# Performance work log

Measured on AMD Instinct MI355X. Metric: run time of the kernel, lower is better.

## Reference

```python
import jax, jax.numpy as jnp
import numpy as np

P, V, GRID = 64, 6890, 32
V_SUB = 256          # vertex subsample for the SDF-grid proxy
SCALE_FACTOR = 0.2   # forward() default
SDF_BAND = 0.15      # proxy: phi = relu(band - dist_to_surface) >= 0
N_FACES = 13776


def _trilinear(vol, pts):
    """torch grid_sample 3D, mode=bilinear, padding=zeros, align_corners=False.
    vol: [D,H,W]; pts: [...,3] with (x,y,z) in [-1,1] mapping to (W,H,D)."""
    D, H, W = vol.shape
    x = ((pts[..., 0] + 1.0) * W - 1.0) * 0.5
    y = ((pts[..., 1] + 1.0) * H - 1.0) * 0.5
    z = ((pts[..., 2] + 1.0) * D - 1.0) * 0.5
    x0 = jnp.floor(x).astype(jnp.int32); fx = x - x0
    y0 = jnp.floor(y).astype(jnp.int32); fy = y - y0
    z0 = jnp.floor(z).astype(jnp.int32); fz = z - z0

    def corner(xi, yi, zi, w):
        inb = (xi >= 0) & (xi < W) & (yi >= 0) & (yi < H) & (zi >= 0) & (zi < D)
        v = vol[jnp.clip(zi, 0, D - 1), jnp.clip(yi, 0, H - 1), jnp.clip(xi, 0, W - 1)]
        return jnp.where(inb, v, 0.0) * w

    return (corner(x0,     y0,     z0,     (1 - fx) * (1 - fy) * (1 - fz))
          + corner(x0 + 1, y0,     z0,     fx       * (1 - fy) * (1 - fz))
          + corner(x0,     y0 + 1, z0,     (1 - fx) * fy       * (1 - fz))
          + corner(x0 + 1, y0 + 1, z0,     fx       * fy       * (1 - fz))
          + corner(x0,     y0,     z0 + 1, (1 - fx) * (1 - fy) * fz)
          + corner(x0 + 1, y0,     z0 + 1, fx       * (1 - fy) * fz)
          + corner(x0,     y0 + 1, z0 + 1, (1 - fx) * fy       * fz)
          + corner(x0 + 1, y0 + 1, z0 + 1, fx       * fy       * fz))


def _compute_phi(verts_cs):
    """Deterministic non-negative SDF-grid proxy (stands in for the external
    SDF CUDA op; original computes it under no_grad). verts_cs: [P,V,3] in [-1,1].
    Returns phi: [P,GRID,GRID,GRID] (D,H,W indexing)."""
    # cell centers in normalized coords (align_corners=False convention)
    lin = (2.0 * jnp.arange(GRID, dtype=verts_cs.dtype) + 1.0) / GRID - 1.0
    zz, yy, xx = jnp.meshgrid(lin, lin, lin, indexing='ij')
    gp = jnp.stack([xx, yy, zz], axis=-1).reshape(-1, 3)  # [G^3,3] (x,y,z)
    stride = V // V_SUB
    sub = verts_cs[:, ::stride, :][:, :V_SUB]             # [P,V_SUB,3]

    def per_person(v):  # v: [V_SUB,3]
        d2 = jnp.sum((gp[:, None, :] - v[None, :, :]) ** 2, axis=-1)  # [G^3,V_SUB]
        d = jnp.sqrt(jnp.min(d2, axis=-1))
        return jnp.maximum(SDF_BAND - d, 0.0).reshape(GRID, GRID, GRID)

    return jax.lax.map(per_person, sub)  # sequential over people: bounds peak memory


def _forward(vertices, translation):
    sg = jax.lax.stop_gradient
    verts = vertices + translation[:, None, :]                      # [P,V,3]
    n = verts.shape[0]
    bmin = sg(jnp.min(verts, axis=1))                               # [P,3] (no_grad bboxes)
    bmax = sg(jnp.max(verts, axis=1))
    # overlap(i,j) per axis: not (min_i > max_j or min_j > max_i)
    ov = jnp.all((bmin[:, None, :] <= bmax[None, :, :]) &
                 (bmin[None, :, :] <= bmax[:, None, :]), axis=-1)   # [P,P], diag True
    # faithful to original ~filter_isolated_boxes: kept only if overlapping ALL others
    valid = jnp.all(ov, axis=1)                                     # [P]
    nv = jnp.sum(valid.astype(verts.dtype))
    center = (bmin + bmax) * 0.5                                    # [P,3]
    scale = (1.0 + SCALE_FACTOR) * 0.5 * jnp.max(bmax - bmin, axis=-1)  # [P]
    verts_cs = sg((verts - center[:, None, :]) / scale[:, None, None])
    phi = sg(_compute_phi(verts_cs))                                # [P,G,G,G]
    # coordinates of ALL people's vertices in person-i's grid frame: [P,P,V,3]
    loc = (verts[None, :, :, :] - center[:, None, None, :]) / scale[:, None, None, None]
    phi_val = jax.vmap(_trilinear)(phi, loc.reshape(n, n * V, 3)).reshape(n, n, V)
    # pair (i,j) contributes iff both valid and i != j (weights[i]=0 in the loop)
    pair_w = (valid[:, None] & valid[None, :] & ~jnp.eye(n, dtype=bool)).astype(verts.dtype)
    denom = jnp.maximum(nv, 1.0) ** 2
    return jnp.sum(pair_w * jnp.sum(phi_val, axis=-1)) / denom


def setup_inputs() -> dict:
    key = jax.random.key(0)
    k1, k2, k3 = jax.random.split(key, 3)
    vertices = jax.random.normal(k1, (P, V, 3), dtype=jnp.float32) * 0.2
    translation = jax.random.uniform(k2, (P, 3), dtype=jnp.float32, minval=-0.3, maxval=0.3)
    faces = jax.random.randint(k3, (N_FACES, 3), 0, V, dtype=jnp.int32)
    return {"vertices": vertices, "translation": translation, "faces": faces}


def reference(vertices, translation, faces):
    # faces only feed the external SDF op (replaced by the phi proxy); unused here
    return _forward(vertices, translation)
```

## Files before the change

kernel.cpp:

```cpp
#include <hip/hip_runtime.h>


#define NP 64
#define NVERT 6890
#define NV3 (NVERT*3)
#define GRD 32
#define QDIM 34
#define QPLANE (QDIM*QDIM)
#define QVOL (QDIM*QPLANE)
#define VSUB 256
#define VSTRIDE 26
#define BAND 0.15f
#define PHI_SCALE 64.0f
#define INV_PHI_SCALE 0.015625f
#define LDS_BYTES (QVOL*2 + 64)
#define SAMPLE_BLOCKS (4*NP)

typedef float floatx2 __attribute__((ext_vector_type(2)));

__device__ __forceinline__ float wave_min(float v) {
  #pragma unroll
  for (int off = 32; off > 0; off >>= 1) v = fminf(v, __shfl_down(v, off));
  return v;
}
__device__ __forceinline__ float wave_max(float v) {
  #pragma unroll
  for (int off = 32; off > 0; off >>= 1) v = fmaxf(v, __shfl_down(v, off));
  return v;
}
__device__ __forceinline__ float wave_sum(float v) {
  #pragma unroll
  for (int off = 32; off > 0; off >>= 1) v += __shfl_down(v, off);
  return v;
}

__global__ __launch_bounds__(1024) void k_soa_bounds(
    const float* __restrict__ verts, const float* __restrict__ trans,
    float* __restrict__ vertsT, float* __restrict__ bbox,
    float* __restrict__ accp, unsigned int* __restrict__ donep) {
  int p = blockIdx.x;
  int tid = threadIdx.x;
  if (p == 0 && tid == 0) { accp[0] = 0.0f; donep[0] = 0u; }
  const float* vp = verts + (size_t)p * NV3;
  float tx = trans[p*3+0], ty = trans[p*3+1], tz = trans[p*3+2];
  float* o0 = vertsT + (size_t)(p*3+0) * NVERT;
  float* o1 = vertsT + (size_t)(p*3+1) * NVERT;
  float* o2 = vertsT + (size_t)(p*3+2) * NVERT;
  float mnx=1e30f, mny=1e30f, mnz=1e30f, mxx=-1e30f, mxy=-1e30f, mxz=-1e30f;
  for (int t2 = tid; t2 < NVERT/2; t2 += 1024) {
    const float* b = vp + t2*6;
    floatx2 A = *(const floatx2*)(b);
    floatx2 B = *(const floatx2*)(b+2);
    floatx2 C = *(const floatx2*)(b+4);
    mnx=fminf(mnx,fminf(A.x,B.y)); mxx=fmaxf(mxx,fmaxf(A.x,B.y));
    mny=fminf(mny,fminf(A.y,C.x)); mxy=fmaxf(mxy,fmaxf(A.y,C.x));
    mnz=fminf(mnz,fminf(B.x,C.y)); mxz=fmaxf(mxz,fmaxf(B.x,C.y));
    floatx2 sx = {A.x+tx, B.y+tx};
    floatx2 sy = {A.y+ty, C.x+ty};
    floatx2 sz = {B.x+tz, C.y+tz};
    *(floatx2*)(o0 + 2*t2) = sx;
    *(floatx2*)(o1 + 2*t2) = sy;
    *(floatx2*)(o2 + 2*t2) = sz;
  }
  mnx=wave_min(mnx)+tx; mny=wave_min(mny)+ty; mnz=wave_min(mnz)+tz;
  mxx=wave_max(mxx)+tx; mxy=wave_max(mxy)+ty; mxz=wave_max(mxz)+tz;
  __shared__ float s[16][6];
  int wave = tid >> 6, lane = tid & 63;
  if (lane == 0) {
    s[wave][0]=mnx; s[wave][1]=mny; s[wave][2]=mnz;
    s[wave][3]=mxx; s[wave][4]=mxy; s[wave][5]=mxz;
  }
  __syncthreads();
  if (tid == 0) {
    float a0=s[0][0],a1=s[0][1],a2=s[0][2],b0=s[0][3],b1=s[0][4],b2=s[0][5];
    for (int w = 1; w < 16; ++w) {
      a0=fminf(a0,s[w][0]); a1=fminf(a1,s[w][1]); a2=fminf(a2,s[w][2]);
      b0=fmaxf(b0,s[w][3]); b1=fmaxf(b1,s[w][4]); b2=fmaxf(b2,s[w][5]);
    }
    bbox[p*3+0]=a0; bbox[p*3+1]=a1; bbox[p*3+2]=a2;
    bbox[192+p*3+0]=b0; bbox[192+p*3+1]=b1; bbox[192+p*3+2]=b2;
  }
}

__global__ __launch_bounds__(1024) void k_phi(
    const float* __restrict__ verts, const float* __restrict__ trans,
    const float* __restrict__ bbox, unsigned short* __restrict__ pairs,
    float* __restrict__ centerg,
    float* __restrict__ validg, int* __restrict__ jlistg,
    int* __restrict__ jcountg, float* __restrict__ nvg) {
  int p = blockIdx.x >> 2;
  int zq = blockIdx.x & 3;
  int tid = threadIdx.x;
  int x = tid & 31, y = tid >> 5;

  __shared__ float kv[VSUB][3];
  __shared__ float phib[8][32][32];
  __shared__ int nkeep;

  const float inv = 1.0f / (float)GRD;
  if (tid == 0) nkeep = 0;
  __syncthreads();

  float bx0 = bbox[p*3+0], by0 = bbox[p*3+1], bz0 = bbox[p*3+2];
  float bx1 = bbox[192+p*3+0], by1 = bbox[192+p*3+1], bz1 = bbox[192+p*3+2];
  float cx = 0.5f*(bx0+bx1), cy = 0.5f*(by0+by1), cz = 0.5f*(bz0+bz1);
  float ext = fmaxf(bx1-bx0, fmaxf(by1-by0, bz1-bz0));
  float is = 1.0f / (0.6f * ext);

  if (zq == 0 && tid == 0) {
    centerg[p*4+0] = cx; centerg[p*4+1] = cy; centerg[p*4+2] = cz;
    centerg[p*4+3] = is * 16.0f;
  }
  if (blockIdx.x == 0 && tid < 64) {
    bool valid = true;
    for (int j = 0; j < NP; ++j) {
      bool ov = true;
      #pragma unroll
      for (int c = 0; c < 3; ++c)
        ov = ov && (bbox[tid*3+c] <= bbox[192+j*3+c]) &&
                   (bbox[j*3+c] <= bbox[192+tid*3+c]);
      valid = valid && ov;
    }
    unsigned long long mm = __ballot(valid);
    if (valid) {
      int pos = (int)__popcll(mm & ((1ull << tid) - 1ull));
      jlistg[pos] = tid;
    }
    validg[tid] = valid ? 1.0f : 0.0f;
    if (tid == 0) {
      jcountg[0] = (int)__popcll(mm);
      nvg[0] = (float)__popcll(mm);
    }
  }

  if (tid < VSUB) {
    int v = tid * VSTRIDE;
    const float* vp = verts + (size_t)p * NV3 + (size_t)v * 3;
    float X = (vp[0] + trans[p*3+0] - cx) * is;
    float Y = (vp[1] + trans[p*3+1] - cy) * is;
    float Z = (vp[2] + trans[p*3+2] - cz) * is;
    float zlo = (2.0f*(zq*8)     + 1.0f) * inv - 1.0f;
    float zhi = (2.0f*(zq*8 + 7) + 1.0f) * inv - 1.0f;
    float dz = fmaxf(fmaxf(zlo - Z, Z - zhi), 0.0f);
    if (dz < BAND) {
      int idx = atomicAdd(&nkeep, 1);
      kv[idx][0] = X; kv[idx][1] = Y; kv[idx][2] = Z;
    }
  }
  __syncthreads();
  int nk = nkeep;

  float gx = (2.0f*x + 1.0f) * inv - 1.0f;
  float gy = (2.0f*y + 1.0f) * inv - 1.0f;
  float gz[8];
  #pragma unroll
  for (int k = 0; k < 8; ++k) gz[k] = (2.0f*(zq*8+k) + 1.0f) * inv - 1.0f;

  float d2[8];
  #pragma unroll
  for (int k = 0; k < 8; ++k) d2[k] = 1e30f;

  int w = tid >> 6;
  float ylo = (4.0f*w + 1.0f) * inv - 1.0f;
  float yhi = (4.0f*w + 3.0f) * inv - 1.0f;

  for (int v = 0; v < nk; ++v) {
    float Y = kv[v][1];
    if (fmaxf(ylo - Y, Y - yhi) >= BAND) continue;
    float dx = gx - kv[v][0];
    float dy = gy - Y;
    float vzv = kv[v][2];
    float r2 = fmaf(dy, dy, dx*dx);
    #pragma unroll
    for (int k = 0; k < 8; ++k) {
      float dz = gz[k] - vzv;
      d2[k] = fminf(d2[k], fmaf(dz, dz, r2));
    }
  }
  #pragma unroll
  for (int k = 0; k < 8; ++k)
    phib[k][y][x] = fmaxf(BAND - sqrtf(d2[k]), 0.0f) * PHI_SCALE;
  __syncthreads();

  unsigned short* qp = pairs + (size_t)p * QVOL;
  for (int idx = tid; idx < QPLANE; idx += 1024) {
    int iy = idx / QDIM, ix = idx % QDIM;
    int gyy = iy - 1, gxx = ix - 1;
    bool gyok = (unsigned)gyy < 32u;
    bool aok = gyok && ((unsigned)gxx < 32u);
    bool bok = gyok && ((unsigned)ix  < 32u);
    int ya = gyok ? gyy : 0;
    int xa = aok ? gxx : 0;
    int xb = bok ? ix : 0;
    #pragma unroll
    for (int k = 0; k < 8; ++k) {
      float a = aok ? phib[k][ya][xa] : 0.0f;
      float b = bok ? phib[k][ya][xb] : 0.0f;
      int pk = __builtin_amdgcn_cvt_pk_fp8_f32(a, b, 0, false);
      qp[(zq*8 + k + 1)*QPLANE + idx] = (unsigned short)(pk & 0xffff);
    }
    if (zq == 0) qp[idx] = 0;
    if (zq == 3) qp[33*QPLANE + idx] = 0;
  }
}

__device__ __forceinline__ float qsample(const unsigned short* q,
                                         float X, float Y, float Z) {
  X = fminf(fmaxf(X, 0.0f), 33.99f);
  Y = fminf(fmaxf(Y, 0.0f), 32.999f);
  Z = fminf(fmaxf(Z, 0.0f), 32.999f);
  float xf = floorf(X), yf = floorf(Y), zf = floorf(Z);
  float fx = X - xf, fy = Y - yf, fz = Z - zf;
  int e = ((int)zf * QDIM + (int)yf) * QDIM + (int)xf;
  unsigned int w00 = q[e];
  unsigned int w10 = q[e + QDIM];
  unsigned int w01 = q[e + QPLANE];
  unsigned int w11 = q[e + QPLANE + QDIM];
  floatx2 c00 = __builtin_amdgcn_cvt_pk_f32_fp8((int)w00, false);
  floatx2 c10 = __builtin_amdgcn_cvt_pk_f32_fp8((int)w10, false);
  floatx2 c01 = __builtin_amdgcn_cvt_pk_f32_fp8((int)w01, false);
  floatx2 c11 = __builtin_amdgcn_cvt_pk_f32_fp8((int)w11, false);
  float u00 = fmaf(fx, c00.y - c00.x, c00.x);
  float u10 = fmaf(fx, c10.y - c10.x, c10.x);
  float u01 = fmaf(fx, c01.y - c01.x, c01.x);
  float u11 = fmaf(fx, c11.y - c11.x, c11.x);
  float a0 = fmaf(fy, u10 - u00, u00);
  float a1 = fmaf(fy, u11 - u01, u01);
  return fmaf(fz, a1 - a0, a0);
}

__global__ __launch_bounds__(896, 7) void k_sample(
    const float* __restrict__ vertsT, const float* __restrict__ centerg,
    const float* __restrict__ validg, const unsigned short* __restrict__ pairs,
    const int* __restrict__ jlistg, const int* __restrict__ jcountg,
    const float* __restrict__ nvg, float* __restrict__ accp,
    unsigned int* __restrict__ donep, float* __restrict__ out) {
  extern __shared__ unsigned char smem[];
  const unsigned short* sq = (const unsigned short*)smem;
  float* red = (float*)(smem + (size_t)QVOL * 2);

  int i = blockIdx.y;
  int tid = threadIdx.x;
  int njl = jcountg[0];

  if (validg[i] != 0.0f) {
    {
      const uint4* src = (const uint4*)(pairs + (size_t)i * QVOL);
      uint4* dst = (uint4*)smem;
      for (int t = tid; t < QVOL/8; t += 896) dst[t] = src[t];
    }
    __syncthreads();

    int v0 = blockIdx.x * 1792 + tid;
    int v1 = v0 + 896;
    bool ok1 = v1 < NVERT;
    int vc1 = ok1 ? v1 : 0;
    float s16 = centerg[i*4+3];
    float bx  = fmaf(-centerg[i*4+0], s16, 16.5f);
    float by  = fmaf(-centerg[i*4+1], s16, 16.5f);
    float bz  = fmaf(-centerg[i*4+2], s16, 16.5f);
    float bx1 = bx + (ok1 ? 0.0f : 1e9f);

    float acc = 0.0f;
    #pragma unroll 2
    for (int t = 0; t < njl; ++t) {
      int jj = jlistg[t];
      if (jj == i) continue;
      const float* p0 = vertsT + (size_t)(jj*3) * NVERT;
      float Xa = fmaf(p0[v0],          s16, bx);
      float Ya = fmaf(p0[NVERT+v0],    s16, by);
      float Za = fmaf(p0[2*NVERT+v0],  s16, bz);
      float Xb = fmaf(p0[vc1],         s16, bx1);
      float Yb = fmaf(p0[NVERT+vc1],   s16, by);
      float Zb = fmaf(p0[2*NVERT+vc1], s16, bz);
      acc += qsample(sq, Xa, Ya, Za);
      acc += qsample(sq, Xb, Yb, Zb);
    }

    acc = wave_sum(acc);
    int wv = tid >> 6, lane = tid & 63;
    if (lane == 0) red[wv] = acc;
    __syncthreads();
    if (tid == 0) {
      float tot = 0.0f;
      #pragma unroll
      for (int w = 0; w < 14; ++w) tot += red[w];
      atomicAdd(accp, tot * INV_PHI_SCALE);
    }
  }

  if (tid == 0) {
    __threadfence();
    unsigned int old = atomicAdd(donep, 1u);
    if (old == SAMPLE_BLOCKS - 1) {
      float nv = fmaxf(nvg[0], 1.0f);
      float loss = atomicAdd(accp, 0.0f);
      out[0] = loss / (nv * nv);
    }
  }
}

extern "C" void kernel_launch(void* const* d_in, const int* in_sizes, int n_in,
                              void* d_out, int out_size, void* d_ws, size_t ws_size,
                              hipStream_t stream) {
  const float* verts = (const float*)d_in[0];
  const float* trans = (const float*)d_in[1];
  float* out = (float*)d_out;

  unsigned short* pairs = (unsigned short*)d_ws;
  float* vertsT    = (float*)((unsigned char*)d_ws + (size_t)NP * QVOL * 2);
  float* bbox      = vertsT + (size_t)NP * NV3;
  float* centerg   = bbox + 384;
  float* validg    = centerg + NP*4;
  float* nvg       = validg + NP;
  float* accp      = nvg + 1;
  unsigned int* donep = (unsigned int*)(accp + 1);
  int* jlistg      = (int*)(donep + 1);
  int* jcountg     = jlistg + NP;

  hipFuncSetAttribute((const void*)k_sample,
                      hipFuncAttributeMaxDynamicSharedMemorySize, LDS_BYTES);

  k_soa_bounds<<<NP, 1024, 0, stream>>>(verts, trans, vertsT, bbox, accp, donep);
  k_phi<<<NP*4, 1024, 0, stream>>>(verts, trans, bbox, pairs, centerg,
                                   validg, jlistg, jcountg, nvg);
  k_sample<<<dim3(4, NP), 896, LDS_BYTES, stream>>>(vertsT, centerg, validg,
                                                    pairs, jlistg, jcountg,
                                                    nvg, accp, donep, out);
}
```

Baseline: 103.2 us.

## Pack 2x2 xy-quads of fp8 phi per dword to halve LDS gathers

The phi grid is now stored as one 32-bit word per cell holding the fp8 values of the 2x2 xy neighbourhood, instead of 16-bit x-pairs. Each trilinear sample therefore needs two LDS loads instead of four. k_phi is split into 8 z-slabs of 4 planes per person rather than 4 slabs of 8 planes. The cost is double the LDS footprint (about 157KB per block) and a doubled global staging copy, and the occupancy hint is dropped from the launch bounds.

```diff
diff --git a/kernel.cpp b/kernel.cpp
--- a/kernel.cpp
+++ b/kernel.cpp
@@ -13,7 +13,7 @@
 #define BAND 0.15f
 #define PHI_SCALE 64.0f
 #define INV_PHI_SCALE 0.015625f
-#define LDS_BYTES (QVOL*2 + 64)
+#define LDS_BYTES (QVOL*4 + 64)
 #define SAMPLE_BLOCKS (4*NP)
 
 typedef float floatx2 __attribute__((ext_vector_type(2)));
@@ -84,17 +84,17 @@
 
 __global__ __launch_bounds__(1024) void k_phi(
     const float* __restrict__ verts, const float* __restrict__ trans,
-    const float* __restrict__ bbox, unsigned short* __restrict__ pairs,
+    const float* __restrict__ bbox, unsigned int* __restrict__ quad,
     float* __restrict__ centerg,
     float* __restrict__ validg, int* __restrict__ jlistg,
     int* __restrict__ jcountg, float* __restrict__ nvg) {
-  int p = blockIdx.x >> 2;
-  int zq = blockIdx.x & 3;
+  int p = blockIdx.x >> 3;
+  int zq = blockIdx.x & 7;
   int tid = threadIdx.x;
   int x = tid & 31, y = tid >> 5;
 
   __shared__ float kv[VSUB][3];
-  __shared__ float phib[8][32][32];
+  __shared__ float phib[4][32][32];
   __shared__ int nkeep;
 
   const float inv = 1.0f / (float)GRD;
@@ -139,8 +139,8 @@
     float X = (vp[0] + trans[p*3+0] - cx) * is;
     float Y = (vp[1] + trans[p*3+1] - cy) * is;
     float Z = (vp[2] + trans[p*3+2] - cz) * is;
-    float zlo = (2.0f*(zq*8)     + 1.0f) * inv - 1.0f;
-    float zhi = (2.0f*(zq*8 + 7) + 1.0f) * inv - 1.0f;
+    float zlo = (2.0f*(zq*4)     + 1.0f) * inv - 1.0f;
+    float zhi = (2.0f*(zq*4 + 3) + 1.0f) * inv - 1.0f;
     float dz = fmaxf(fmaxf(zlo - Z, Z - zhi), 0.0f);
     if (dz < BAND) {
       int idx = atomicAdd(&nkeep, 1);
@@ -152,13 +152,13 @@
 
   float gx = (2.0f*x + 1.0f) * inv - 1.0f;
   float gy = (2.0f*y + 1.0f) * inv - 1.0f;
-  float gz[8];
-  #pragma unroll
-  for (int k = 0; k < 8; ++k) gz[k] = (2.0f*(zq*8+k) + 1.0f) * inv - 1.0f;
-
-  float d2[8];
-  #pragma unroll
-  for (int k = 0; k < 8; ++k) d2[k] = 1e30f;
+  float gz[4];
+  #pragma unroll
+  for (int k = 0; k < 4; ++k) gz[k] = (2.0f*(zq*4+k) + 1.0f) * inv - 1.0f;
+
+  float d2[4];
+  #pragma unroll
+  for (int k = 0; k < 4; ++k) d2[k] = 1e30f;
 
   int w = tid >> 6;
   float ylo = (4.0f*w + 1.0f) * inv - 1.0f;
@@ -172,72 +172,70 @@
     float vzv = kv[v][2];
     float r2 = fmaf(dy, dy, dx*dx);
     #pragma unroll
-    for (int k = 0; k < 8; ++k) {
+    for (int k = 0; k < 4; ++k) {
       float dz = gz[k] - vzv;
       d2[k] = fminf(d2[k], fmaf(dz, dz, r2));
     }
   }
   #pragma unroll
-  for (int k = 0; k < 8; ++k)
+  for (int k = 0; k < 4; ++k)
     phib[k][y][x] = fmaxf(BAND - sqrtf(d2[k]), 0.0f) * PHI_SCALE;
   __syncthreads();
 
-  unsigned short* qp = pairs + (size_t)p * QVOL;
+  unsigned int* qp = quad + (size_t)p * QVOL;
   for (int idx = tid; idx < QPLANE; idx += 1024) {
     int iy = idx / QDIM, ix = idx % QDIM;
     int gyy = iy - 1, gxx = ix - 1;
-    bool gyok = (unsigned)gyy < 32u;
-    bool aok = gyok && ((unsigned)gxx < 32u);
-    bool bok = gyok && ((unsigned)ix  < 32u);
-    int ya = gyok ? gyy : 0;
-    int xa = aok ? gxx : 0;
-    int xb = bok ? ix : 0;
+    bool x0ok = (unsigned)gxx < 32u, x1ok = (unsigned)ix < 32u;
+    bool y0ok = (unsigned)gyy < 32u, y1ok = (unsigned)iy < 32u;
+    int xa = x0ok ? gxx : 0, xb = x1ok ? ix : 0;
+    int ya = y0ok ? gyy : 0, yb = y1ok ? iy : 0;
     #pragma unroll
-    for (int k = 0; k < 8; ++k) {
-      float a = aok ? phib[k][ya][xa] : 0.0f;
-      float b = bok ? phib[k][ya][xb] : 0.0f;
-      int pk = __builtin_amdgcn_cvt_pk_fp8_f32(a, b, 0, false);
-      qp[(zq*8 + k + 1)*QPLANE + idx] = (unsigned short)(pk & 0xffff);
-    }
-    if (zq == 0) qp[idx] = 0;
-    if (zq == 3) qp[33*QPLANE + idx] = 0;
-  }
-}
-
-__device__ __forceinline__ float qsample(const unsigned short* q,
+    for (int k = 0; k < 4; ++k) {
+      float a = (x0ok && y0ok) ? phib[k][ya][xa] : 0.0f;
+      float b = (x1ok && y0ok) ? phib[k][ya][xb] : 0.0f;
+      float c = (x0ok && y1ok) ? phib[k][yb][xa] : 0.0f;
+      float d = (x1ok && y1ok) ? phib[k][yb][xb] : 0.0f;
+      int lo = __builtin_amdgcn_cvt_pk_fp8_f32(a, b, 0, false);
+      int wd = __builtin_amdgcn_cvt_pk_fp8_f32(c, d, lo, true);
+      qp[(zq*4 + k + 1)*QPLANE + idx] = (unsigned int)wd;
+    }
+    if (zq == 0) qp[idx] = 0u;
+    if (zq == 7) qp[33*QPLANE + idx] = 0u;
+  }
+}
+
+__device__ __forceinline__ float qsample(const unsigned char* sq,
                                          float X, float Y, float Z) {
   X = fminf(fmaxf(X, 0.0f), 33.99f);
-  Y = fminf(fmaxf(Y, 0.0f), 32.999f);
+  Y = fminf(fmaxf(Y, 0.0f), 33.99f);
   Z = fminf(fmaxf(Z, 0.0f), 32.999f);
   float xf = floorf(X), yf = floorf(Y), zf = floorf(Z);
   float fx = X - xf, fy = Y - yf, fz = Z - zf;
   int e = ((int)zf * QDIM + (int)yf) * QDIM + (int)xf;
-  unsigned int w00 = q[e];
-  unsigned int w10 = q[e + QDIM];
-  unsigned int w01 = q[e + QPLANE];
-  unsigned int w11 = q[e + QPLANE + QDIM];
-  floatx2 c00 = __builtin_amdgcn_cvt_pk_f32_fp8((int)w00, false);
-  floatx2 c10 = __builtin_amdgcn_cvt_pk_f32_fp8((int)w10, false);
-  floatx2 c01 = __builtin_amdgcn_cvt_pk_f32_fp8((int)w01, false);
-  floatx2 c11 = __builtin_amdgcn_cvt_pk_f32_fp8((int)w11, false);
-  float u00 = fmaf(fx, c00.y - c00.x, c00.x);
-  float u10 = fmaf(fx, c10.y - c10.x, c10.x);
-  float u01 = fmaf(fx, c01.y - c01.x, c01.x);
-  float u11 = fmaf(fx, c11.y - c11.x, c11.x);
-  float a0 = fmaf(fy, u10 - u00, u00);
-  float a1 = fmaf(fy, u11 - u01, u01);
-  return fmaf(fz, a1 - a0, a0);
-}
-
-__global__ __launch_bounds__(896, 7) void k_sample(
+  unsigned int w0 = *(const unsigned int*)(sq + e*4);
+  unsigned int w1 = *(const unsigned int*)(sq + e*4 + QPLANE*4);
+  floatx2 l0 = __builtin_amdgcn_cvt_pk_f32_fp8((int)w0, false);
+  floatx2 h0 = __builtin_amdgcn_cvt_pk_f32_fp8((int)w0, true);
+  floatx2 l1 = __builtin_amdgcn_cvt_pk_f32_fp8((int)w1, false);
+  floatx2 h1 = __builtin_amdgcn_cvt_pk_f32_fp8((int)w1, true);
+  float u0 = fmaf(fx, l0.y - l0.x, l0.x);
+  float u1 = fmaf(fx, h0.y - h0.x, h0.x);
+  float vA = fmaf(fy, u1 - u0, u0);
+  float u2 = fmaf(fx, l1.y - l1.x, l1.x);
+  float u3 = fmaf(fx, h1.y - h1.x, h1.x);
+  float vB = fmaf(fy, u3 - u2, u2);
+  return fmaf(fz, vB - vA, vA);
+}
+
+__global__ __launch_bounds__(896) void k_sample(
     const float* __restrict__ vertsT, const float* __restrict__ centerg,
-    const float* __restrict__ validg, const unsigned short* __restrict__ pairs,
+    const float* __restrict__ validg, const unsigned int* __restrict__ quad,
     const int* __restrict__ jlistg, const int* __restrict__ jcountg,
     const float* __restrict__ nvg, float* __restrict__ accp,
     unsigned int* __restrict__ donep, float* __restrict__ out) {
   extern __shared__ unsigned char smem[];
-  const unsigned short* sq = (const unsigned short*)smem;
-  float* red = (float*)(smem + (size_t)QVOL * 2);
+  float* red = (float*)(smem + (size_t)QVOL * 4);
 
   int i = blockIdx.y;
   int tid = threadIdx.x;
@@ -245,9 +243,9 @@
 
   if (validg[i] != 0.0f) {
     {
-      const uint4* src = (const uint4*)(pairs + (size_t)i * QVOL);
+      const uint4* src = (const uint4*)(quad + (size_t)i * QVOL);
       uint4* dst = (uint4*)smem;
-      for (int t = tid; t < QVOL/8; t += 896) dst[t] = src[t];
+      for (int t = tid; t < QVOL/4; t += 896) dst[t] = src[t];
     }
     __syncthreads();
 
@@ -273,8 +271,8 @@
       float Xb = fmaf(p0[vc1],         s16, bx1);
       float Yb = fmaf(p0[NVERT+vc1],   s16, by);
       float Zb = fmaf(p0[2*NVERT+vc1], s16, bz);
-      acc += qsample(sq, Xa, Ya, Za);
-      acc += qsample(sq, Xb, Yb, Zb);
+      acc += qsample(smem, Xa, Ya, Za);
+      acc += qsample(smem, Xb, Yb, Zb);
     }
 
     acc = wave_sum(acc);
@@ -307,8 +305,8 @@
   const float* trans = (const float*)d_in[1];
   float* out = (float*)d_out;
 
-  unsigned short* pairs = (unsigned short*)d_ws;
-  float* vertsT    = (float*)((unsigned char*)d_ws + (size_t)NP * QVOL * 2);
+  unsigned int* quad = (unsigned int*)d_ws;
+  float* vertsT    = (float*)d_ws + (size_t)NP * QVOL;
   float* bbox      = vertsT + (size_t)NP * NV3;
   float* centerg   = bbox + 384;
   float* validg    = centerg + NP*4;
@@ -322,9 +320,9 @@
                       hipFuncAttributeMaxDynamicSharedMemorySize, LDS_BYTES);
 
   k_soa_bounds<<<NP, 1024, 0, stream>>>(verts, trans, vertsT, bbox, accp, donep);
-  k_phi<<<NP*4, 1024, 0, stream>>>(verts, trans, bbox, pairs, centerg,
+  k_phi<<<NP*8, 1024, 0, stream>>>(verts, trans, bbox, quad, centerg,
                                    validg, jlistg, jcountg, nvg);
   k_sample<<<dim3(4, NP), 896, LDS_BYTES, stream>>>(vertsT, centerg, validg,
-                                                    pairs, jlistg, jcountg,
+                                                    quad, jlistg, jcountg,
                                                     nvg, accp, donep, out);
 }
```

After: 104.2 us. About the same (+1.0%).
